# Optimization experiments

Hardware: AMD Instinct MI355X
Metric: run time of the kernel (lower is better)

Reference implementation:

```python
import jax, jax.numpy as jnp
import numpy as np

DIM = 1024
HEADS = 16
DIM_HEAD = 64
INNER = HEADS * DIM_HEAD  # 1024
SCALE = DIM_HEAD ** -0.5


def setup_inputs() -> dict:
    key = jax.random.key(0)
    k_x, k_qkv, k_ow, k_ob = jax.random.split(key, 4)
    B, N = 4, 2048
    x = jax.random.normal(k_x, (B, N, DIM), dtype=jnp.float32)
    # nn.Linear weights stored as [out, in] in torch; keep [in, out] for x @ W.
    w_qkv = jax.random.normal(k_qkv, (DIM, 3 * INNER), dtype=jnp.float32) * (DIM ** -0.5)
    w_out = jax.random.normal(k_ow, (INNER, DIM), dtype=jnp.float32) * (INNER ** -0.5)
    b_out = jax.random.normal(k_ob, (DIM,), dtype=jnp.float32) * 0.01
    return {"x": x, "w_qkv": w_qkv, "w_out": w_out, "b_out": b_out}


def reference(x, w_qkv, w_out, b_out):
    B, N, _ = x.shape
    qkv = x @ w_qkv  # [B, N, 3*inner]
    q, k, v = jnp.split(qkv, 3, axis=-1)
    # [B, N, inner] -> [B, H, N, dh]
    def to_heads(t):
        return t.reshape(B, N, HEADS, DIM_HEAD).transpose(0, 2, 1, 3)
    q, k, v = to_heads(q), to_heads(k), to_heads(v)
    attn = jnp.einsum("bhqd,bhkd->bhqk", q, k) * SCALE  # [B, H, N, N]
    attn = jax.nn.softmax(attn, axis=-1)
    out = jnp.einsum("bhqk,bhkd->bhqd", attn, v)  # [B, H, N, dh]
    out = out.transpose(0, 2, 1, 3).reshape(B, N, INNER)
    return out @ w_out + b_out
```

## Files before the change

### kernel.cpp

```cpp
#include <hip/hip_runtime.h>
#include <hip/hip_bf16.h>
#include <stdint.h>

typedef __attribute__((ext_vector_type(4))) float f32x4;
typedef __attribute__((ext_vector_type(16))) float f32x16;
typedef __attribute__((ext_vector_type(8))) short s16x8;
typedef __attribute__((ext_vector_type(4))) short s16x4;
typedef __attribute__((ext_vector_type(4))) unsigned int u32x4;

#define DEV static __device__ __forceinline__

constexpr int B_ = 4, H_ = 16, N_ = 2048;
constexpr float CL_ = 0.18033688011112042f;

DEV short f2bf(float x) {
  __hip_bfloat16 h = __float2bfloat16(x);
  return *reinterpret_cast<short*>(&h);
}

DEV uint32_t cvtpk(float lo, float hi) {
  uint32_t r;
  asm("v_cvt_pk_bf16_f32 %0, %1, %2" : "=v"(r) : "v"(lo), "v"(hi));
  return r;
}

DEV void gload16(const void* g, void* l) {
  __builtin_amdgcn_global_load_lds((const __attribute__((address_space(1))) void*)g,
                                   (__attribute__((address_space(3))) void*)l, 16, 0, 0);
}

__global__ void k_prep(const float* __restrict__ x, short* __restrict__ xb,
                       const float* __restrict__ wqkv, short* __restrict__ wqkvT,
                       const float* __restrict__ wout, short* __restrict__ woutT) {
  __shared__ short t[64][72];
  int bid = blockIdx.x, tid = threadIdx.x;
  if (bid < 4096) {
    int i = (bid * 256 + tid) * 8;
    const float4* p = reinterpret_cast<const float4*>(x + i);
    float4 a = p[0], b = p[1];
    s16x8 o;
    o[0] = f2bf(a.x); o[1] = f2bf(a.y); o[2] = f2bf(a.z); o[3] = f2bf(a.w);
    o[4] = f2bf(b.x); o[5] = f2bf(b.y); o[6] = f2bf(b.z); o[7] = f2bf(b.w);
    *reinterpret_cast<s16x8*>(xb + i) = o;
    return;
  }
  const float* W;
  short* WT;
  int R = 1024, C, r0, c0;
  if (bid < 4864) {
    int id = bid - 4096;
    W = wqkv; WT = wqkvT; C = 3072;
    c0 = (id % 48) * 64; r0 = (id / 48) * 64;
  } else {
    int id = bid - 4864;
    W = wout; WT = woutT; C = 1024;
    c0 = (id % 16) * 64; r0 = (id / 16) * 64;
  }
  int r = tid >> 2, cp = (tid & 3) * 16;
  const float4* s4 = reinterpret_cast<const float4*>(W + (size_t)(r0 + r) * C + c0 + cp);
  float4 f0 = s4[0], f1 = s4[1], f2 = s4[2], f3 = s4[3];
  short* tr = &t[r][cp];
  tr[0] = f2bf(f0.x); tr[1] = f2bf(f0.y); tr[2]  = f2bf(f0.z); tr[3]  = f2bf(f0.w);
  tr[4] = f2bf(f1.x); tr[5] = f2bf(f1.y); tr[6]  = f2bf(f1.z); tr[7]  = f2bf(f1.w);
  tr[8] = f2bf(f2.x); tr[9] = f2bf(f2.y); tr[10] = f2bf(f2.z); tr[11] = f2bf(f2.w);
  tr[12] = f2bf(f3.x); tr[13] = f2bf(f3.y); tr[14] = f2bf(f3.z); tr[15] = f2bf(f3.w);
  __syncthreads();
  int cc = tid >> 2, rp = (tid & 3) * 16;
  short buf[16];
#pragma unroll
  for (int i = 0; i < 16; ++i) buf[i] = t[rp + i][cc];
  short* dst = WT + (size_t)(c0 + cc) * R + r0 + rp;
  *reinterpret_cast<s16x8*>(dst) = *reinterpret_cast<s16x8*>(buf);
  *reinterpret_cast<s16x8*>(dst + 8) = *reinterpret_cast<s16x8*>(buf + 8);
}

__global__ void k_tv(const short* __restrict__ v, short* __restrict__ vT) {
  __shared__ short t[64][72];
  int bh = blockIdx.y, n0 = blockIdx.x * 64;
  int tid = threadIdx.x;
  int r = tid >> 2, cp = (tid & 3) * 16;
  const short* src = v + ((size_t)bh * N_ + n0 + r) * 64 + cp;
  *reinterpret_cast<s16x8*>(&t[r][cp]) = *reinterpret_cast<const s16x8*>(src);
  *reinterpret_cast<s16x8*>(&t[r][cp + 8]) = *reinterpret_cast<const s16x8*>(src + 8);
  __syncthreads();
  int d = tid >> 2, np = (tid & 3) * 16;
  short buf[16];
#pragma unroll
  for (int i = 0; i < 16; ++i) buf[i] = t[np + i][d];
  short* dst = vT + ((size_t)bh * 64 + d) * N_ + n0 + np;
  *reinterpret_cast<s16x8*>(dst) = *reinterpret_cast<s16x8*>(buf);
  *reinterpret_cast<s16x8*>(dst + 8) = *reinterpret_cast<s16x8*>(buf + 8);
}

template <int EPI>
__global__ __launch_bounds__(256, 2)
void k_gemm(const short* __restrict__ A, const short* __restrict__ BT,
            int M, int N, int K,
            short* __restrict__ oq, short* __restrict__ ok, short* __restrict__ ov,
            const float* __restrict__ bias, float* __restrict__ out) {
  __shared__ short As[128 * 32];
  __shared__ short Bs[128 * 32];
  const int tid = threadIdx.x;
  const int m0 = blockIdx.x * 128, n0 = blockIdx.y * 128;
  const int lane = tid & 63, w = tid >> 6, g = lane >> 4, c = lane & 15;
  const int wr = w >> 1, wc = w & 1;
  f32x4 acc[4][4] = {};
  const int trow = tid >> 2, tk = (tid & 3) * 8;
  const short* ga = A + (size_t)(m0 + trow) * K + tk;
  const short* gb = BT + (size_t)(n0 + trow) * K + tk;
  short* la = As + tid * 8;
  short* lb = Bs + tid * 8;
  for (int k0 = 0; k0 < K; k0 += 32) {
    gload16(ga + k0, la);
    gload16(ga + (size_t)64 * K + k0, la + 2048);
    gload16(gb + k0, lb);
    gload16(gb + (size_t)64 * K + k0, lb + 2048);
    __syncthreads();
    s16x8 af[4], bf[4];
#pragma unroll
    for (int i = 0; i < 4; ++i)
      af[i] = *reinterpret_cast<const s16x8*>(As + (wr * 64 + i * 16 + c) * 32 + g * 8);
#pragma unroll
    for (int j = 0; j < 4; ++j)
      bf[j] = *reinterpret_cast<const s16x8*>(Bs + (wc * 64 + j * 16 + c) * 32 + g * 8);
#pragma unroll
    for (int i = 0; i < 4; ++i)
#pragma unroll
      for (int j = 0; j < 4; ++j)
        acc[i][j] = __builtin_amdgcn_mfma_f32_16x16x32_bf16(af[i], bf[j], acc[i][j], 0, 0, 0);
    __syncthreads();
  }
  if (EPI == 0) {
#pragma unroll
    for (int bj = 0; bj < 4; ++bj) {
      int ncol = n0 + wc * 64 + bj * 16 + c;
      int part = ncol >> 10;
      int c10 = ncol & 1023;
      int h = c10 >> 6, d = c10 & 63;
      short* dst0 = part == 0 ? oq : (part == 1 ? ok : ov);
      float qs = (part == 0) ? CL_ : 1.0f;
#pragma unroll
      for (int ai = 0; ai < 4; ++ai) {
#pragma unroll
        for (int r = 0; r < 4; ++r) {
          int mrow = m0 + wr * 64 + ai * 16 + g * 4 + r;
          int b = mrow >> 11, nr = mrow & 2047;
          dst0[((size_t)((b * H_ + h) * N_ + nr) << 6) + d] = f2bf(acc[ai][bj][r] * qs);
        }
      }
    }
  } else {
#pragma unroll
    for (int bj = 0; bj < 4; ++bj) {
      int ncol = n0 + wc * 64 + bj * 16 + c;
      float bb = bias[ncol];
#pragma unroll
      for (int ai = 0; ai < 4; ++ai) {
#pragma unroll
        for (int r = 0; r < 4; ++r) {
          int mrow = m0 + wr * 64 + ai * 16 + g * 4 + r;
          out[(size_t)mrow * N + ncol] = acc[ai][bj][r] + bb;
        }
      }
    }
  }
}

__global__ __launch_bounds__(256, 4)
void k_attn(const short* __restrict__ q, const short* __restrict__ kk,
            const short* __restrict__ vT, short* __restrict__ ao) {
  __shared__ __align__(16) char smem[32768];
  constexpr int NT = N_ / 64;
  int bh = blockIdx.x, qb = blockIdx.y;
  int b = bh >> 4, head = bh & 15;
  int tid = threadIdx.x, w = tid >> 6, lane = tid & 63;
  int half = lane >> 5, qc = lane & 31;
  const size_t ho = (size_t)bh * (N_ * 64);
  const short* Q = q + ho;
  const char* Kc = reinterpret_cast<const char*>(kk + ho);
  const char* Vc = reinterpret_cast<const char*>(vT + ho);
  int q0w = qb * 128 + w * 32;
  s16x8 qf[4];
#pragma unroll
  for (int ks = 0; ks < 4; ++ks)
    qf[ks] = *reinterpret_cast<const s16x8*>(Q + (size_t)(q0w + qc) * 64 + ks * 16 + half * 8);
  f32x16 ot[2] = {};
  float lp0 = 0.f, lp1 = 0.f, lp2 = 0.f, lp3 = 0.f;
  const int rsw0 = ((qc ^ (qc >> 3)) & 7) << 4;
  const int rsw1 = rsw0 ^ 0x40;
  const int s_i0 = tid, s_i1 = tid + 256;
  const int s_r0 = s_i0 >> 3, s_r1 = s_i1 >> 3;
  const int s_c0 = (((s_i0 & 7) ^ ((s_r0 ^ (s_r0 >> 3)) & 7)) << 4);
  const int s_c1 = (((s_i1 & 7) ^ ((s_r1 ^ (s_r1 >> 3)) & 7)) << 4);
#define STAGE(T)                                                                       \
  {                                                                                    \
    char* nb = smem + ((T) & 1) * 16384;                                               \
    gload16(Kc + (size_t)((T) * 64 + s_r0) * 128 + s_c0, nb + s_i0 * 16);              \
    gload16(Kc + (size_t)((T) * 64 + s_r1) * 128 + s_c1, nb + s_i1 * 16);              \
    gload16(Vc + (size_t)s_r0 * 4096 + (T) * 128 + s_c0, nb + 8192 + s_i0 * 16);       \
    gload16(Vc + (size_t)s_r1 * 4096 + (T) * 128 + s_c1, nb + 8192 + s_i1 * 16);       \
  }
  STAGE(0);
  __syncthreads();
  for (int tt = 0; tt < NT; ++tt) {
    if (tt + 1 < NT) STAGE(tt + 1);
    const char* kb_ = smem + (tt & 1) * 16384;
    const char* vb_ = kb_ + 8192;
    f32x16 st[2];
#pragma unroll
    for (int j = 0; j < 2; ++j) {
      const int rs = j ? rsw1 : rsw0;
      s16x8 kfj[4];
#pragma unroll
      for (int ks = 0; ks < 4; ++ks)
        kfj[ks] = *reinterpret_cast<const s16x8*>(kb_ + (j * 32 + qc) * 128 + ((ks * 32 + half * 16) ^ rs));
      f32x16 acc = {};
      __builtin_amdgcn_s_setprio(1);
#pragma unroll
      for (int ks = 0; ks < 4; ++ks)
        acc = __builtin_amdgcn_mfma_f32_32x32x16_bf16(kfj[ks], qf[ks], acc, 0, 0, 0);
      __builtin_amdgcn_s_setprio(0);
      st[j] = acc;
    }
#pragma unroll
    for (int j = 0; j < 2; ++j)
#pragma unroll
      for (int r = 0; r < 16; ++r) {
        float p = __builtin_amdgcn_exp2f(st[j][r]);
        st[j][r] = p;
        if ((r & 3) == 0) lp0 += p;
        else if ((r & 3) == 1) lp1 += p;
        else if ((r & 3) == 2) lp2 += p;
        else lp3 += p;
      }
    u32x4 pwv[4];
#pragma unroll
    for (int j = 0; j < 2; ++j)
#pragma unroll
      for (int bb = 0; bb < 2; ++bb)
#pragma unroll
        for (int p = 0; p < 2; ++p) {
          uint32_t Aw = cvtpk(st[j][8 * bb + 2 * p], st[j][8 * bb + 2 * p + 1]);
          uint32_t Bw = cvtpk(st[j][8 * bb + 4 + 2 * p], st[j][8 * bb + 4 + 2 * p + 1]);
          asm volatile("v_permlane32_swap_b32 %0, %1" : "+v"(Aw), "+v"(Bw));
          pwv[j * 2 + bb][p] = Aw;
          pwv[j * 2 + bb][p + 2] = Bw;
        }
#pragma unroll
    for (int db = 0; db < 2; ++db) {
      const int rs = db ? rsw1 : rsw0;
      s16x8 vf[4];
#pragma unroll
      for (int kb4 = 0; kb4 < 4; ++kb4)
        vf[kb4] = *reinterpret_cast<const s16x8*>(vb_ + (db * 32 + qc) * 128 + ((kb4 * 32 + half * 16) ^ rs));
      f32x16 acc = ot[db];
      __builtin_amdgcn_s_setprio(1);
#pragma unroll
      for (int kb4 = 0; kb4 < 4; ++kb4)
        acc = __builtin_amdgcn_mfma_f32_32x32x16_bf16(
            vf[kb4], __builtin_bit_cast(s16x8, pwv[kb4]), acc, 0, 0, 0);
      __builtin_amdgcn_s_setprio(0);
      ot[db] = acc;
    }
    __syncthreads();
  }
#undef STAGE
  float lp = (lp0 + lp1) + (lp2 + lp3);
  float linv = 1.f / (lp + __shfl_xor(lp, 32, 64));
  short* Oq = reinterpret_cast<short*>(smem) + w * 2304;
#pragma unroll
  for (int db = 0; db < 2; ++db)
#pragma unroll
    for (int m = 0; m < 4; ++m) {
      uint2 pk;
      pk.x = cvtpk(ot[db][4 * m] * linv, ot[db][4 * m + 1] * linv);
      pk.y = cvtpk(ot[db][4 * m + 2] * linv, ot[db][4 * m + 3] * linv);
      *reinterpret_cast<uint2*>(Oq + qc * 72 + db * 32 + m * 8 + half * 4) = pk;
    }
  int q2 = lane >> 1, dcol = (lane & 1) * 32;
  size_t ro = (size_t)(b * N_ + q0w + q2) * 1024 + head * 64 + dcol;
#pragma unroll
  for (int ch = 0; ch < 4; ++ch) {
    s16x8 vv = *reinterpret_cast<const s16x8*>(Oq + q2 * 72 + dcol + ch * 8);
    *reinterpret_cast<s16x8*>(ao + ro + ch * 8) = vv;
  }
}

extern "C" void kernel_launch(void* const* d_in, const int* in_sizes, int n_in,
                              void* d_out, int out_size, void* d_ws, size_t ws_size,
                              hipStream_t stream) {
  const float* x = (const float*)d_in[0];
  const float* w_qkv = (const float*)d_in[1];
  const float* w_out = (const float*)d_in[2];
  const float* b_out = (const float*)d_in[3];
  float* out = (float*)d_out;
  char* ws = (char*)d_ws;
  short* xb    = (short*)(ws);
  short* wqkvT = (short*)(ws + 16777216);
  short* woutT = (short*)(ws + 23068672);
  short* qB    = (short*)(ws + 25165824);
  short* kB    = (short*)(ws + 41943040);
  short* vtmp  = (short*)(ws + 58720256);
  short* vTT   = (short*)(ws + 75497472);
  short* ao    = xb;

  k_prep<<<5120, 256, 0, stream>>>(x, xb, w_qkv, wqkvT, w_out, woutT);
  k_gemm<0><<<dim3(64, 24), 256, 0, stream>>>(xb, wqkvT, 8192, 3072, 1024,
                                              qB, kB, vtmp, nullptr, nullptr);
  k_tv<<<dim3(32, 64), 256, 0, stream>>>(vtmp, vTT);
  k_attn<<<dim3(64, 16), 256, 0, stream>>>(qB, kB, vTT, ao);
  k_gemm<1><<<dim3(64, 8), 256, 0, stream>>>(ao, woutT, 8192, 1024, 1024,
                                             nullptr, nullptr, nullptr, b_out, out);
}
```

Measured before the change: 196.8 us.

## Pipeline QKV GEMM with multi-stage LDS buffering and fuse V transpose into epilogue

Replaces the QKV projection GEMM with a 512-thread, 128x256-tile kernel that prefetches K-slices two steps ahead into a 4-slot LDS ring, using waitcnt and raw barriers instead of double syncthreads per step. The V part of the epilogue now writes directly in transposed [bh, d, n] layout with packed bf16 stores, removing the separate transpose kernel and its round-trip through global memory. The larger tile and 96KB of shared memory may reduce occupancy, and the transposed V stores are strided per lane.

```diff
diff --git a/kernel.cpp b/kernel.cpp
--- a/kernel.cpp
+++ b/kernel.cpp
@@ -74,30 +74,91 @@
   *reinterpret_cast<s16x8*>(dst + 8) = *reinterpret_cast<s16x8*>(buf + 8);
 }
 
-__global__ void k_tv(const short* __restrict__ v, short* __restrict__ vT) {
-  __shared__ short t[64][72];
-  int bh = blockIdx.y, n0 = blockIdx.x * 64;
-  int tid = threadIdx.x;
-  int r = tid >> 2, cp = (tid & 3) * 16;
-  const short* src = v + ((size_t)bh * N_ + n0 + r) * 64 + cp;
-  *reinterpret_cast<s16x8*>(&t[r][cp]) = *reinterpret_cast<const s16x8*>(src);
-  *reinterpret_cast<s16x8*>(&t[r][cp + 8]) = *reinterpret_cast<const s16x8*>(src + 8);
-  __syncthreads();
-  int d = tid >> 2, np = (tid & 3) * 16;
-  short buf[16];
-#pragma unroll
-  for (int i = 0; i < 16; ++i) buf[i] = t[np + i][d];
-  short* dst = vT + ((size_t)bh * 64 + d) * N_ + n0 + np;
-  *reinterpret_cast<s16x8*>(dst) = *reinterpret_cast<s16x8*>(buf);
-  *reinterpret_cast<s16x8*>(dst + 8) = *reinterpret_cast<s16x8*>(buf + 8);
-}
-
-template <int EPI>
+__global__ __launch_bounds__(512, 2)
+void k_gemm0(const short* __restrict__ A, const short* __restrict__ BT,
+             short* __restrict__ oq, short* __restrict__ ok, short* __restrict__ ovT) {
+  __shared__ __align__(16) char smem[98304];
+  constexpr int NT = 32;
+  const int tid = threadIdx.x;
+  const int m0 = blockIdx.x * 128, n0 = blockIdx.y * 256;
+  const int lane = tid & 63, w = tid >> 6, g = (lane >> 4) & 3, c = lane & 15;
+  const int wm = w & 1, wn = w >> 1;
+  f32x4 acc[4][4] = {};
+  const int ra = tid >> 2, ca = (tid & 3) * 8;
+  const int rb1 = ra + 128;
+  const short* gA = A + (size_t)(m0 + ra) * 1024 + ca;
+  const short* gB0 = BT + (size_t)(n0 + ra) * 1024 + ca;
+  const short* gB1 = BT + (size_t)(n0 + rb1) * 1024 + ca;
+#define STAGE0(T)                                                   \
+  {                                                                 \
+    char* nb = smem + ((T) & 3) * 24576;                            \
+    gload16(gA + (T) * 32, nb + tid * 16);                          \
+    gload16(gB0 + (T) * 32, nb + 8192 + tid * 16);                  \
+    gload16(gB1 + (T) * 32, nb + 8192 + (tid + 512) * 16);          \
+  }
+  STAGE0(0);
+  STAGE0(1);
+  for (int t = 0; t < NT; ++t) {
+    if (t + 1 < NT) {
+      asm volatile("s_waitcnt vmcnt(3)" ::: "memory");
+    } else {
+      asm volatile("s_waitcnt vmcnt(0)" ::: "memory");
+    }
+    __builtin_amdgcn_s_barrier();
+    __builtin_amdgcn_sched_barrier(0);
+    if (t + 2 < NT) STAGE0(t + 2);
+    const char* sb = smem + (t & 3) * 24576;
+    s16x8 af[4], bf[4];
+#pragma unroll
+    for (int i = 0; i < 4; ++i)
+      af[i] = *reinterpret_cast<const s16x8*>(sb + (wm * 64 + i * 16 + c) * 64 + g * 16);
+#pragma unroll
+    for (int j = 0; j < 4; ++j)
+      bf[j] = *reinterpret_cast<const s16x8*>(sb + 8192 + (wn * 64 + j * 16 + c) * 64 + g * 16);
+    __builtin_amdgcn_s_setprio(1);
+#pragma unroll
+    for (int i = 0; i < 4; ++i)
+#pragma unroll
+      for (int j = 0; j < 4; ++j)
+        acc[i][j] = __builtin_amdgcn_mfma_f32_16x16x32_bf16(af[i], bf[j], acc[i][j], 0, 0, 0);
+    __builtin_amdgcn_s_setprio(0);
+  }
+#undef STAGE0
+#pragma unroll
+  for (int j = 0; j < 4; ++j) {
+    int ncol = n0 + wn * 64 + j * 16 + c;
+    int part = ncol >> 10;
+    int c10 = ncol & 1023;
+    int h = c10 >> 6, d = c10 & 63;
+    if (part == 2) {
+#pragma unroll
+      for (int i = 0; i < 4; ++i) {
+        int mrow = m0 + wm * 64 + i * 16 + g * 4;
+        int b = mrow >> 11, nr = mrow & 2047;
+        uint2 pk;
+        pk.x = cvtpk(acc[i][j][0], acc[i][j][1]);
+        pk.y = cvtpk(acc[i][j][2], acc[i][j][3]);
+        *reinterpret_cast<uint2*>(ovT + ((size_t)((b * H_ + h) * 64 + d) * N_ + nr)) = pk;
+      }
+    } else {
+      short* dst0 = (part == 0) ? oq : ok;
+      float qs = (part == 0) ? CL_ : 1.0f;
+#pragma unroll
+      for (int i = 0; i < 4; ++i) {
+#pragma unroll
+        for (int r = 0; r < 4; ++r) {
+          int mrow = m0 + wm * 64 + i * 16 + g * 4 + r;
+          int b = mrow >> 11, nr = mrow & 2047;
+          dst0[((size_t)((b * H_ + h) * N_ + nr) << 6) + d] = f2bf(acc[i][j][r] * qs);
+        }
+      }
+    }
+  }
+}
+
 __global__ __launch_bounds__(256, 2)
-void k_gemm(const short* __restrict__ A, const short* __restrict__ BT,
-            int M, int N, int K,
-            short* __restrict__ oq, short* __restrict__ ok, short* __restrict__ ov,
-            const float* __restrict__ bias, float* __restrict__ out) {
+void k_gemm1(const short* __restrict__ A, const short* __restrict__ BT,
+             int M, int N, int K, const float* __restrict__ bias, float* __restrict__ out) {
   __shared__ short As[128 * 32];
   __shared__ short Bs[128 * 32];
   const int tid = threadIdx.x;
@@ -130,37 +191,16 @@
         acc[i][j] = __builtin_amdgcn_mfma_f32_16x16x32_bf16(af[i], bf[j], acc[i][j], 0, 0, 0);
     __syncthreads();
   }
-  if (EPI == 0) {
-#pragma unroll
-    for (int bj = 0; bj < 4; ++bj) {
-      int ncol = n0 + wc * 64 + bj * 16 + c;
-      int part = ncol >> 10;
-      int c10 = ncol & 1023;
-      int h = c10 >> 6, d = c10 & 63;
-      short* dst0 = part == 0 ? oq : (part == 1 ? ok : ov);
-      float qs = (part == 0) ? CL_ : 1.0f;
-#pragma unroll
-      for (int ai = 0; ai < 4; ++ai) {
-#pragma unroll
-        for (int r = 0; r < 4; ++r) {
-          int mrow = m0 + wr * 64 + ai * 16 + g * 4 + r;
-          int b = mrow >> 11, nr = mrow & 2047;
-          dst0[((size_t)((b * H_ + h) * N_ + nr) << 6) + d] = f2bf(acc[ai][bj][r] * qs);
-        }
-      }
-    }
-  } else {
-#pragma unroll
-    for (int bj = 0; bj < 4; ++bj) {
-      int ncol = n0 + wc * 64 + bj * 16 + c;
-      float bb = bias[ncol];
-#pragma unroll
-      for (int ai = 0; ai < 4; ++ai) {
-#pragma unroll
-        for (int r = 0; r < 4; ++r) {
-          int mrow = m0 + wr * 64 + ai * 16 + g * 4 + r;
-          out[(size_t)mrow * N + ncol] = acc[ai][bj][r] + bb;
-        }
+#pragma unroll
+  for (int bj = 0; bj < 4; ++bj) {
+    int ncol = n0 + wc * 64 + bj * 16 + c;
+    float bb = bias[ncol];
+#pragma unroll
+    for (int ai = 0; ai < 4; ++ai) {
+#pragma unroll
+      for (int r = 0; r < 4; ++r) {
+        int mrow = m0 + wr * 64 + ai * 16 + g * 4 + r;
+        out[(size_t)mrow * N + ncol] = acc[ai][bj][r] + bb;
       }
     }
   }
@@ -300,15 +340,11 @@
   short* woutT = (short*)(ws + 23068672);
   short* qB    = (short*)(ws + 25165824);
   short* kB    = (short*)(ws + 41943040);
-  short* vtmp  = (short*)(ws + 58720256);
   short* vTT   = (short*)(ws + 75497472);
   short* ao    = xb;
 
   k_prep<<<5120, 256, 0, stream>>>(x, xb, w_qkv, wqkvT, w_out, woutT);
-  k_gemm<0><<<dim3(64, 24), 256, 0, stream>>>(xb, wqkvT, 8192, 3072, 1024,
-                                              qB, kB, vtmp, nullptr, nullptr);
-  k_tv<<<dim3(32, 64), 256, 0, stream>>>(vtmp, vTT);
+  k_gemm0<<<dim3(64, 12), 512, 0, stream>>>(xb, wqkvT, qB, kB, vTT);
   k_attn<<<dim3(64, 16), 256, 0, stream>>>(qB, kB, vTT, ao);
-  k_gemm<1><<<dim3(64, 8), 256, 0, stream>>>(ao, woutT, 8192, 1024, 1024,
-                                             nullptr, nullptr, nullptr, b_out, out);
-}
+  k_gemm1<<<dim3(64, 8), 256, 0, stream>>>(ao, woutT, 8192, 1024, 1024, b_out, out);
+}
```

New measurement: 191.1 us. -2.9%, faster.
